# Kernel tuning notes

Hardware: AMD Instinct MI355X
Metric: run time of the kernel (lower is better)

The kernel has to match this reference:

```python
import jax, jax.numpy as jnp
import numpy as np

T, L, B, M, E, H, A, HID, OBS = 8, 2, 512, 128, 512, 8, 16, 1024, 64
DH = E // H


def _ln(x, s, b):
    m = jnp.mean(x, axis=-1, keepdims=True)
    v = jnp.var(x, axis=-1, keepdims=True)
    return (x - m) * jax.lax.rsqrt(v + 1e-6) * s + b


def _mlp(z, w1, b1, w2, b2, w3, b3):
    z = jax.nn.relu(z @ w1 + b1)
    z = jax.nn.relu(z @ w2 + b2)
    return z @ w3 + b3


def setup_inputs() -> dict:
    key = jax.random.key(0)
    ks = jax.random.split(key, 20)
    r = lambda i, shape: jax.random.normal(ks[i], shape, jnp.float32) * 0.02
    return dict(
        memories=jax.random.normal(ks[0], (B, L, M, E), jnp.float32),
        obs=jax.random.normal(ks[1], (B, OBS), jnp.float32),
        We=r(2, (T, OBS, E)), be=jnp.zeros((T, E), jnp.float32),
        Wq=r(3, (T, L, E, E)), Wk=r(4, (T, L, E, E)), Wv=r(5, (T, L, E, E)),
        Wo=r(6, (T, L, E, E)), bo=jnp.zeros((T, L, E), jnp.float32),
        W1=r(7, (T, L, E, E)), b1=jnp.zeros((T, L, E), jnp.float32),
        W2=r(8, (T, L, E, E)), b2=jnp.zeros((T, L, E), jnp.float32),
        ln1_s=jnp.ones((T, L, E), jnp.float32), ln1_b=jnp.zeros((T, L, E), jnp.float32),
        ln2_s=jnp.ones((T, L, E), jnp.float32), ln2_b=jnp.zeros((T, L, E), jnp.float32),
        aW1=r(9, (T, E, HID)), ab1=jnp.zeros((T, HID), jnp.float32),
        aW2=r(10, (T, HID, HID)), ab2=jnp.zeros((T, HID), jnp.float32),
        aW3=r(11, (T, HID, A)), ab3=jnp.zeros((T, A), jnp.float32),
        cW1=r(12, (T, E, HID)), cb1=jnp.zeros((T, HID), jnp.float32),
        cW2=r(13, (T, HID, HID)), cb2=jnp.zeros((T, HID), jnp.float32),
        cW3=r(14, (T, HID, 1)), cb3=jnp.zeros((T, 1), jnp.float32),
        state_skills=jax.random.randint(ks[15], (B,), 0, T),
        mask=jnp.ones((B, M), dtype=bool),
    )


def reference(memories, obs, We, be, Wq, Wk, Wv, Wo, bo, W1, b1, W2, b2,
              ln1_s, ln1_b, ln2_s, ln2_b, aW1, ab1, aW2, ab2, aW3, ab3,
              cW1, cb1, cW2, cb2, cW3, cb3, state_skills, mask):
    scale = 1.0 / np.sqrt(DH)
    # current-step token is always attendable -> append True column
    fmask = jnp.concatenate([mask, jnp.ones((B, 1), dtype=bool)], axis=1)  # [B, M+1]
    xs, mems = [], []
    for t in range(T):  # dense compute over ALL tasks (as in the original)
        h = obs @ We[t] + be[t]  # [B, E]
        layer_mems = []
        for l in range(L):
            layer_mems.append(h)  # TrXL-style: memory_out = layer inputs
            kv = jnp.concatenate([memories[:, l], h[:, None, :]], axis=1)  # [B, M+1, E]
            qn = _ln(h, ln1_s[t, l], ln1_b[t, l])
            kn = _ln(kv, ln1_s[t, l], ln1_b[t, l])
            q = (qn @ Wq[t, l]).reshape(B, H, DH)
            k = (kn @ Wk[t, l]).reshape(B, M + 1, H, DH)
            v = (kn @ Wv[t, l]).reshape(B, M + 1, H, DH)
            s = jnp.einsum('bhd,bshd->bhs', q, k) * scale
            s = jnp.where(fmask[:, None, :], s, -1e9)
            p = jax.nn.softmax(s, axis=-1)
            o = jnp.einsum('bhs,bshd->bhd', p, v).reshape(B, E) @ Wo[t, l] + bo[t, l]
            h = h + o
            hn = _ln(h, ln2_s[t, l], ln2_b[t, l])
            h = h + jax.nn.relu(hn @ W1[t, l] + b1[t, l]) @ W2[t, l] + b2[t, l]
        xs.append(h)
        mems.append(jnp.stack(layer_mems, axis=1))  # [B, L, E]
    x_all = jnp.stack(xs, axis=1)       # [B, T, E]
    mem_all = jnp.stack(mems, axis=1)   # [B, T, L, E]
    onehot = jnp.eye(T, dtype=x_all.dtype)[state_skills]  # [B, T]
    x = jnp.sum(x_all * onehot[:, :, None], axis=1)                 # [B, E]
    memory_out = jnp.sum(mem_all * onehot[:, :, None, None], axis=1)  # [B, L, E]
    actor = jnp.stack([_mlp(x, aW1[t], ab1[t], aW2[t], ab2[t], aW3[t], ab3[t]) for t in range(T)], axis=1)   # [B, T, A]
    critic = jnp.stack([_mlp(x, cW1[t], cb1[t], cW2[t], cb2[t], cW3[t], cb3[t]) for t in range(T)], axis=1)  # [B, T, 1]
    logits = jnp.sum(actor * onehot[:, :, None], axis=1)                    # [B, A]
    values = jnp.sum(critic * onehot[:, :, None], axis=1).squeeze(-1)       # [B]
    return logits, values, memory_out
```

## Files before the change

kernel.cpp:

```cpp
#include <hip/hip_runtime.h>

#define TT    8
#define LLAY  2
#define BB    512
#define MM    128
#define EE    512
#define NH    8
#define HID   1024
#define NA    16
#define NOBS  64

#define OUT_LOGITS 0
#define OUT_VALUES (BB*NA)
#define OUT_MEM    (BB*NA + BB)

#define WS_H    0
#define WS_R    (WS_H + BB*EE)
#define WS_B16  (WS_R + BB*NH*EE)
#define U_QN    0
#define U_HN    (U_QN + BB*EE)
#define U_F1    (U_HN + BB*EE)
#define U_O     (U_F1 + BB*EE)
#define U_HB    (U_O  + BB*EE)
#define U_PV    (U_HB + BB*EE)
#define U_Z1A   (U_PV + BB*NH*EE)
#define U_Z2A   (U_Z1A + BB*HID)
#define U_Z1C   (U_Z2A + BB*HID)
#define U_Z2C   (U_Z1C + BB*HID)
#define U_OBSB  (U_Z2C + BB*HID)
#define U_QB    (U_OBSB + BB*NOBS)
#define U_END   (U_QB + BB*EE)
#define WS_INT  (WS_B16 + (U_END + 1)/2)

#define WI_CNT  0
#define WI_OFF  8
#define WI_MODE 17
#define WI_ROWL 32

typedef __attribute__((ext_vector_type(8))) short bf16x8;
typedef __attribute__((ext_vector_type(4))) float f32x4;

__device__ __forceinline__ unsigned short f2bf(float f) {
  unsigned u = __float_as_uint(f);
  unsigned r = (u + 0x7fffu + ((u >> 16) & 1u)) >> 16;
  return (unsigned short)r;
}
__device__ __forceinline__ float bf2f(unsigned short u) {
  return __uint_as_float(((unsigned)u) << 16);
}
__device__ __forceinline__ float bflo(unsigned u) { return __uint_as_float(u << 16); }
__device__ __forceinline__ float bfhi(unsigned u) { return __uint_as_float(u & 0xffff0000u); }

__device__ __forceinline__ unsigned cvt_pk_bf16(float lo, float hi) {
  unsigned r;
  asm("v_cvt_pk_bf16_f32 %0, %1, %2" : "=v"(r) : "v"(lo), "v"(hi));
  return r;
}
__device__ __forceinline__ bf16x8 pack8(const float* f) {
  union { unsigned u[4]; bf16x8 v; } x;
  x.u[0] = cvt_pk_bf16(f[0], f[1]);
  x.u[1] = cvt_pk_bf16(f[2], f[3]);
  x.u[2] = cvt_pk_bf16(f[4], f[5]);
  x.u[3] = cvt_pk_bf16(f[6], f[7]);
  return x.v;
}

#define DPP_ADD(x, ctrl) \
  (x) += __int_as_float(__builtin_amdgcn_update_dpp(0, __float_as_int(x), (ctrl), 0xf, 0xf, true))

__device__ __forceinline__ float wave_sum(float x) {
  DPP_ADD(x, 0x121);
  DPP_ADD(x, 0x122);
  DPP_ADD(x, 0x124);
  DPP_ADD(x, 0x128);
  x += __shfl_xor(x, 16);
  x += __shfl_xor(x, 32);
  return x;
}

__device__ __forceinline__ float f4c(const float4 v, int c) {
  return c == 0 ? v.x : (c == 1 ? v.y : (c == 2 ? v.z : v.w));
}

__global__ __launch_bounds__(256) void prep_k(const int* __restrict__ skills,
                                              const void* __restrict__ mask,
                                              const float* __restrict__ obs,
                                              unsigned short* __restrict__ obsb,
                                              int* __restrict__ wsI)
{
  if (blockIdx.x > 0) {
    const int i = ((blockIdx.x - 1)*256 + threadIdx.x)*4;
    const float4 v = *(const float4*)(obs + i);
    uint2 p;
    p.x = cvt_pk_bf16(v.x, v.y);
    p.y = cvt_pk_bf16(v.z, v.w);
    *(uint2*)(obsb + i) = p;
    return;
  }
  __shared__ int cnt_s[TT];
  __shared__ int off_s[TT];
  const int tid = threadIdx.x;
  if (tid < TT) cnt_s[tid] = 0;
  __syncthreads();
  const int b0 = tid, b1i = tid + 256;
  const int t0 = skills[b0], t1 = skills[b1i];
  const int o0 = atomicAdd(&cnt_s[t0], 1);
  const int o1 = atomicAdd(&cnt_s[t1], 1);
  __syncthreads();
  if (tid == 0) {
    int off = 0;
    for (int t = 0; t < TT; ++t) {
      off_s[t] = off;
      wsI[WI_CNT + t] = cnt_s[t];
      wsI[WI_OFF + t] = off;
      off += cnt_s[t];
    }
    const unsigned char* m8 = (const unsigned char*)mask;
    const int w0 = *(const int*)mask;
    int mode = 0;
    if (m8[0] == 1 && m8[1] == 1 && m8[2] == 1 && m8[3] == 1) mode = 0;
    else if (w0 == 1) mode = 1;
    else if (w0 == 0x3f800000) mode = 2;
    wsI[WI_MODE] = mode;
  }
  __syncthreads();
  wsI[WI_ROWL + off_s[t0] + o0] = b0;
  wsI[WI_ROWL + off_s[t1] + o1] = b1i;
}

template<bool MEMOUT>
__global__ __launch_bounds__(256) void ln_k(const float* __restrict__ src,
                                            unsigned short* __restrict__ dst,
                                            const float* __restrict__ sp,
                                            const float* __restrict__ bp,
                                            const int* __restrict__ skills,
                                            float* __restrict__ memout, int l)
{
  const int b = blockIdx.x, tid = threadIdx.x;
  const int t = skills[b];
  const float x0 = src[(size_t)b*EE + tid];
  const float x1 = src[(size_t)b*EE + tid + 256];
  if (MEMOUT) {
    memout[((size_t)b*LLAY + l)*EE + tid] = x0;
    memout[((size_t)b*LLAY + l)*EE + tid + 256] = x1;
  }
  __shared__ float rs[4], rq[4];
  float s = wave_sum(x0 + x1);
  float q = wave_sum(x0*x0 + x1*x1);
  const int wvi = tid >> 6, lane = tid & 63;
  if (lane == 0) { rs[wvi] = s; rq[wvi] = q; }
  __syncthreads();
  const float S = rs[0] + rs[1] + rs[2] + rs[3];
  const float Q = rq[0] + rq[1] + rq[2] + rq[3];
  const float mu = S * (1.f/EE);
  const float inv = rsqrtf(Q*(1.f/EE) - mu*mu + 1e-6f);
  const size_t pb = ((size_t)t*LLAY + l)*EE;
  dst[(size_t)b*EE + tid]       = f2bf((x0 - mu)*inv*sp[pb + tid]       + bp[pb + tid]);
  dst[(size_t)b*EE + tid + 256] = f2bf((x1 - mu)*inv*sp[pb + tid + 256] + bp[pb + tid + 256]);
}

template<int KK, int KSPLIT, int RF, bool RELU, bool HASBIAS, bool HASRES, bool OUTBF, bool HEADA, bool OUTBOTH>
__global__ __launch_bounds__((KSPLIT == 8) ? 512 : 256) void mg_k(
    const unsigned short* __restrict__ Aa, const unsigned short* __restrict__ Ab, int lda,
    const float* __restrict__ Wa, const float* __restrict__ Wb, long wStride, long wOff,
    int N,
    const float* __restrict__ biasa, const float* __restrict__ biasb, int bStride, int bOff,
    const float* __restrict__ res, int ldres,
    void* __restrict__ Ca, void* __restrict__ Cb_, int ldc,
    unsigned short* __restrict__ C2,
    const int* __restrict__ wsI)
{
  constexpr int NW = (KSPLIT == 8) ? 8 : 4;
  constexpr int Kper = KK / KSPLIT;
  constexpr int NK = Kper / 32;
  constexpr int MR = RF * 16;
  const int t = blockIdx.z & 7, sel = blockIdx.z >> 3;
  const int cnt = wsI[WI_CNT + t];
  if (cnt == 0) return;
  const int* rowl = wsI + WI_ROWL + wsI[WI_OFF + t];
  const int tid = threadIdx.x, lane = tid & 63, w = tid >> 6;
  const int l15 = lane & 15, l4 = lane >> 4;
  const int kw    = (KSPLIT == 8) ? w : (w & 1);
  const int ntile = (KSPLIT == 8) ? 0 : (w >> 1);
  const int jbase = blockIdx.x * (KSPLIT == 8 ? 16 : 32) + ntile*16;

  const unsigned short* A = sel ? Ab : Aa;
  const float* Wt = (sel ? Wb : Wa) + (size_t)t*wStride + wOff;
  const float* wp = Wt + (size_t)(kw*Kper + l4*8)*N + jbase + l15;

  bf16x8 afr[NK];
  #pragma unroll
  for (int kk = 0; kk < NK; ++kk) {
    float f[8];
    #pragma unroll
    for (int j = 0; j < 8; ++j) f[j] = wp[(size_t)(kk*32 + j)*N];
    afr[kk] = pack8(f);
  }

  __shared__ __align__(16) f32x4 red_s[NW][RF][64];

  for (int rb = blockIdx.y*MR; rb < cnt; rb += (int)gridDim.y*MR) {
    int row[RF];
    const unsigned short* ap[RF];
    #pragma unroll
    for (int rf = 0; rf < RF; ++rf) {
      row[rf] = rowl[min(rb + rf*16 + l15, cnt - 1)];
      ap[rf] = A + (size_t)row[rf]*lda
          + (HEADA ? (size_t)(jbase >> 6)*EE : 0) + kw*Kper + l4*8;
    }
    f32x4 acc[RF];
    #pragma unroll
    for (int rf = 0; rf < RF; ++rf) acc[rf] = (f32x4){0.f, 0.f, 0.f, 0.f};

    #pragma unroll
    for (int kk = 0; kk < NK; ++kk) {
      #pragma unroll
      for (int rf = 0; rf < RF; ++rf) {
        const bf16x8 bfr = *(const bf16x8*)(ap[rf] + kk*32);
        acc[rf] = __builtin_amdgcn_mfma_f32_16x16x32_bf16(afr[kk], bfr, acc[rf], 0, 0, 0);
      }
    }

    #pragma unroll
    for (int rf = 0; rf < RF; ++rf) red_s[w][rf][lane] = acc[rf];
    __syncthreads();

    if (kw == 0) {
      #pragma unroll
      for (int rf = 0; rf < RF; ++rf) {
        if (KSPLIT == 8) {
          #pragma unroll
          for (int ww = 1; ww < 8; ++ww) acc[rf] += red_s[ww][rf][lane];
        } else {
          acc[rf] += red_s[w + 1][rf][lane];
        }
        if (rb + rf*16 + l15 < cnt) {
          const int nb = jbase + l4*4;
          float vv[4];
          float4 bv, rv;
          if (HASBIAS) bv = *(const float4*)((sel ? biasb : biasa) + (size_t)t*bStride + bOff + nb);
          if (HASRES)  rv = *(const float4*)(res + (size_t)row[rf]*ldres + nb);
          #pragma unroll
          for (int c = 0; c < 4; ++c) {
            float x = acc[rf][c];
            if (HASBIAS) x += f4c(bv, c);
            if (RELU)    x = fmaxf(x, 0.f);
            if (HASRES)  x += f4c(rv, c);
            vv[c] = x;
          }
          void* C = sel ? Cb_ : Ca;
          if (OUTBF) {
            uint2 p;
            p.x = cvt_pk_bf16(vv[0], vv[1]);
            p.y = cvt_pk_bf16(vv[2], vv[3]);
            *(uint2*)((unsigned short*)C + (size_t)row[rf]*ldc + nb) = p;
          } else {
            *(float4*)((float*)C + (size_t)row[rf]*ldc + nb) = make_float4(vv[0], vv[1], vv[2], vv[3]);
          }
          if (OUTBOTH) {
            uint2 p;
            p.x = cvt_pk_bf16(vv[0], vv[1]);
            p.y = cvt_pk_bf16(vv[2], vv[3]);
            *(uint2*)(C2 + (size_t)row[rf]*ldc + nb) = p;
          }
        }
      }
    }
    __syncthreads();
  }
}

__global__ __launch_bounds__(256) void rk_k(const unsigned short* __restrict__ qb,
                                            const float* __restrict__ Wk,
                                            float* __restrict__ R_ws,
                                            const int* __restrict__ wsI, int l)
{
  const int t = blockIdx.z & 7, h = blockIdx.z >> 3;
  const int cnt = wsI[WI_CNT + t];
  if (cnt == 0) return;
  const int* rowl = wsI + WI_ROWL + wsI[WI_OFF + t];
  const int tid = threadIdx.x, lane = tid & 63, w = tid >> 6;
  const int l15 = lane & 15, l4 = lane >> 4;
  const int kw = w & 1, ntile = w >> 1;
  const int ebase = blockIdx.x*32 + ntile*16;

  const float* wp = Wk + ((size_t)t*LLAY + l)*EE*EE
      + (size_t)(ebase + l15)*EE + h*64 + kw*32 + l4*8;

  __shared__ __align__(16) f32x4 red_s[4][2][64];

  for (int rb = blockIdx.y*32; rb < cnt; rb += (int)gridDim.y*32) {
    int row[2];
    const unsigned short* ap[2];
    #pragma unroll
    for (int rf = 0; rf < 2; ++rf) {
      row[rf] = rowl[min(rb + rf*16 + l15, cnt - 1)];
      ap[rf] = qb + (size_t)row[rf]*EE + h*64 + kw*32 + l4*8;
    }
    float f[8];
    *(float4*)&f[0] = *(const float4*)wp;
    *(float4*)&f[4] = *(const float4*)(wp + 4);
    const bf16x8 afr = pack8(f);
    f32x4 acc[2];
    #pragma unroll
    for (int rf = 0; rf < 2; ++rf) {
      const bf16x8 bfr = *(const bf16x8*)ap[rf];
      acc[rf] = __builtin_amdgcn_mfma_f32_16x16x32_bf16(afr, bfr,
                  (f32x4){0.f,0.f,0.f,0.f}, 0, 0, 0);
    }
    #pragma unroll
    for (int rf = 0; rf < 2; ++rf) red_s[w][rf][lane] = acc[rf];
    __syncthreads();
    if (kw == 0) {
      #pragma unroll
      for (int rf = 0; rf < 2; ++rf) {
        acc[rf] += red_s[w + 1][rf][lane];
        if (rb + rf*16 + l15 < cnt) {
          const int e = ebase + l4*4;
          *(float4*)(R_ws + ((size_t)row[rf]*NH + h)*EE + e) =
              make_float4(acc[rf][0], acc[rf][1], acc[rf][2], acc[rf][3]);
        }
      }
    }
    __syncthreads();
  }
}

__global__ __launch_bounds__(256) void attn_k(const float* __restrict__ mem,
                                              const unsigned short* __restrict__ qn,
                                              const float* __restrict__ R_ws,
                                              const float* __restrict__ ln1s,
                                              const float* __restrict__ ln1b,
                                              const void* __restrict__ mask,
                                              const int* __restrict__ skills,
                                              const int* __restrict__ wsI,
                                              unsigned short* __restrict__ PV, int l)
{
  const int b = blockIdx.x, tid = threadIdx.x;
  const int wvi = tid >> 6, lane = tid & 63;
  const int l15 = lane & 15, l4 = lane >> 4;
  const int t = skills[b];
  const int mode = wsI[WI_MODE];

  __shared__ __align__(16) float qn_l[EE];
  __shared__ __align__(16) float w_s[NH][132];
  __shared__ __align__(16) float p_s[NH][MM];
  __shared__ float mu_s[MM], inv_s[MM], S_s[MM], Q_s[MM];
  __shared__ float hsS[NH], hsA[NH], hsP[NH], hspex[NH];
  __shared__ __align__(16) unsigned short rp_bf[16][520];
  __shared__ __align__(16) float score_s[MM][20];

  for (int i = tid; i < EE; i += 256) qn_l[i] = bf2f(qn[(size_t)b*EE + i]);

  const int e8 = lane*8;
  const float* s1p = ln1s + ((size_t)t*LLAY + l)*EE;
  const float* b1p = ln1b + ((size_t)t*LLAY + l)*EE;
  float s1v[8], b1v[8], qnv[8];
  *(float4*)&s1v[0] = *(const float4*)(s1p + e8);
  *(float4*)&s1v[4] = *(const float4*)(s1p + e8 + 4);
  *(float4*)&b1v[0] = *(const float4*)(b1p + e8);
  *(float4*)&b1v[4] = *(const float4*)(b1p + e8 + 4);
  {
    const uint4 qu = *(const uint4*)(qn + (size_t)b*EE + e8);
    qnv[0] = bflo(qu.x); qnv[1] = bfhi(qu.x);
    qnv[2] = bflo(qu.y); qnv[3] = bfhi(qu.y);
    qnv[4] = bflo(qu.z); qnv[5] = bfhi(qu.z);
    qnv[6] = bflo(qu.w); qnv[7] = bfhi(qu.w);
  }

  const float scale = 0.125f;
  float rp[NH][8];
  float SR[NH], BR[NH], SE[NH];
  #pragma unroll
  for (int h = 0; h < NH; ++h) {
    float rv[8];
    *(float4*)&rv[0] = *(const float4*)(R_ws + ((size_t)b*NH + h)*EE + e8);
    *(float4*)&rv[4] = *(const float4*)(R_ws + ((size_t)b*NH + h)*EE + e8 + 4);
    float pr = 0.f, pb = 0.f, ps = 0.f;
    #pragma unroll
    for (int j = 0; j < 8; ++j) {
      const float r = rv[j]*scale;
      const float x = r*s1v[j];
      rp[h][j] = x;
      pr += x; pb += b1v[j]*r; ps += qnv[j]*r;
    }
    SR[h] = wave_sum(pr);
    BR[h] = wave_sum(pb);
    SE[h] = wave_sum(ps);
  }

  if (wvi == 0) {
    #pragma unroll
    for (int h = 0; h < NH; ++h)
      *(bf16x8*)&rp_bf[h][e8] = pack8(rp[h]);
  } else if (wvi == 1) {
    bf16x8 ones, zer;
    #pragma unroll
    for (int j = 0; j < 8; ++j) { ones[j] = (short)0x3F80; zer[j] = 0; }
    *(bf16x8*)&rp_bf[8][e8] = ones;
    #pragma unroll
    for (int r = 9; r < 16; ++r) *(bf16x8*)&rp_bf[r][e8] = zer;
  }
  if (tid == 0) {
    #pragma unroll
    for (int h = 0; h < NH; ++h) w_s[h][MM] = SE[h];
  }
  __syncthreads();

  const float* base = mem + ((size_t)b*LLAY + l)*MM*EE;
  #pragma unroll
  for (int half = 0; half < 2; ++half) {
    const int mt = wvi + half*4;
    const int mg = mt*16 + l15;
    const float* xp = base + (size_t)mg*EE + l4*8;
    f32x4 sacc = {0.f,0.f,0.f,0.f}, gacc = {0.f,0.f,0.f,0.f};
    #pragma unroll
    for (int ks = 0; ks < 16; ++ks) {
      float f[8];
      *(float4*)&f[0] = *(const float4*)(xp + ks*32);
      *(float4*)&f[4] = *(const float4*)(xp + ks*32 + 4);
      const bf16x8 xfr = pack8(f);
      const bf16x8 afr = *(const bf16x8*)&rp_bf[l15][ks*32 + l4*8];
      sacc = __builtin_amdgcn_mfma_f32_16x16x32_bf16(afr, xfr, sacc, 0, 0, 0);
      gacc = __builtin_amdgcn_mfma_f32_16x16x32_bf16(xfr, xfr, gacc, 0, 0, 0);
    }
    if (l4 < 2) *(f32x4*)&score_s[mg][l4*4] = sacc;
    if (l4 == 2) S_s[mg] = sacc[0];
    if (l4 == (l15 >> 2)) {
      const int c = l15 & 3;
      Q_s[mg] = (c == 0) ? gacc[0] : (c == 1) ? gacc[1] : (c == 2) ? gacc[2] : gacc[3];
    }
  }
  __syncthreads();

  if (tid < MM) {
    const int m = tid;
    const float muv = S_s[m]*(1.f/EE);
    const float invv = rsqrtf(Q_s[m]*(1.f/EE) - muv*muv + 1e-6f);
    mu_s[m] = muv; inv_s[m] = invv;
    bool valid;
    if (mode == 0)      valid = ((const unsigned char*)mask)[(size_t)b*MM + m] != 0;
    else if (mode == 1) valid = ((const int*)mask)[(size_t)b*MM + m] != 0;
    else                valid = ((const float*)mask)[(size_t)b*MM + m] != 0.f;
    #pragma unroll
    for (int h = 0; h < NH; ++h) {
      const float sc = invv*score_s[m][h] - muv*invv*SR[h] + BR[h];
      const float p = valid ? __expf(sc) : 0.f;
      p_s[h][m] = p;
      w_s[h][m] = p*invv;
    }
  }
  __syncthreads();

  {
    const int h = tid >> 5, li = tid & 31;
    const float p0 = p_s[h][li], p1 = p_s[h][li+32], p2 = p_s[h][li+64], p3 = p_s[h][li+96];
    const float i0 = inv_s[li], i1 = inv_s[li+32], i2 = inv_s[li+64], i3 = inv_s[li+96];
    const float m0 = mu_s[li], m1 = mu_s[li+32], m2 = mu_s[li+64], m3 = mu_s[li+96];
    const float pe = (li == 0) ? __expf(w_s[h][MM]) : 0.f;
    float Sp = p0 + p1 + p2 + p3 + pe;
    float Ap = p0*m0*i0 + p1*m1*i1 + p2*m2*i2 + p3*m3*i3;
    float Pp = p0 + p1 + p2 + p3;
    #pragma unroll
    for (int o = 16; o; o >>= 1) {
      Sp += __shfl_xor(Sp, o);
      Ap += __shfl_xor(Ap, o);
      Pp += __shfl_xor(Pp, o);
    }
    if (li == 0) { hsS[h] = Sp; hsA[h] = Ap; hsP[h] = Pp; hspex[h] = pe; }
  }
  __syncthreads();

  const int e0 = wvi*128 + lane*2;
  const float s1x = s1p[e0], s1y = s1p[e0+1];
  const float b1x = b1p[e0], b1y = b1p[e0+1];
  const float qx = qn_l[e0], qy = qn_l[e0+1];
  float accx[NH], accy[NH];
  #pragma unroll
  for (int h = 0; h < NH; ++h) { accx[h] = 0.f; accy[h] = 0.f; }
  const float* bp2 = mem + ((size_t)b*LLAY + l)*MM*EE + e0;
  for (int m4 = 0; m4 < MM; m4 += 4) {
    float4 wv4[NH];
    #pragma unroll
    for (int h = 0; h < NH; ++h) wv4[h] = *(const float4*)&w_s[h][m4];
    #pragma unroll
    for (int c = 0; c < 4; ++c) {
      const float2 x2 = *(const float2*)(bp2 + (size_t)(m4 + c)*EE);
      #pragma unroll
      for (int h = 0; h < NH; ++h) {
        const float wv = f4c(wv4[h], c);
        accx[h] += wv*x2.x;
        accy[h] += wv*x2.y;
      }
    }
  }
  #pragma unroll
  for (int h = 0; h < NH; ++h) {
    const float is = 1.f/hsS[h];
    const float px = (s1x*(accx[h] - hsA[h]) + b1x*hsP[h] + hspex[h]*qx)*is;
    const float py = (s1y*(accy[h] - hsA[h]) + b1y*hsP[h] + hspex[h]*qy)*is;
    const unsigned pk = cvt_pk_bf16(px, py);
    *(unsigned*)(PV + ((size_t)b*NH + h)*EE + e0) = pk;
  }
}

__global__ __launch_bounds__(256) void head_k(const unsigned short* __restrict__ z2a,
                                              const unsigned short* __restrict__ z2c,
                                              const float* __restrict__ aW3,
                                              const float* __restrict__ ab3,
                                              const float* __restrict__ cW3,
                                              const float* __restrict__ cb3,
                                              const int* __restrict__ skills,
                                              float* __restrict__ out)
{
  const int b = blockIdx.x, tid = threadIdx.x;
  const int t = skills[b];
  __shared__ float za[HID], zc[HID];
  __shared__ float red[16][17];
  __shared__ float redv[4];
  for (int i = tid; i < HID; i += 256) {
    za[i] = bf2f(z2a[(size_t)b*HID + i]);
    zc[i] = bf2f(z2c[(size_t)b*HID + i]);
  }
  __syncthreads();
  {
    const int j = tid & 15, grp = tid >> 4;
    const float* w = aW3 + (size_t)t*HID*NA;
    float p = 0.f;
    for (int i = grp*64; i < grp*64 + 64; ++i) p += za[i]*w[(size_t)i*NA + j];
    red[grp][j] = p;
  }
  float pvv = 0.f;
  {
    const float* w = cW3 + (size_t)t*HID;
    for (int i = tid; i < HID; i += 256) pvv += zc[i]*w[i];
  }
  pvv = wave_sum(pvv);
  const int wvi = tid >> 6, lane = tid & 63;
  if (lane == 0) redv[wvi] = pvv;
  __syncthreads();
  if (tid < 16) {
    float v = ab3[(size_t)t*NA + tid];
    #pragma unroll
    for (int g = 0; g < 16; ++g) v += red[g][tid];
    out[OUT_LOGITS + (size_t)b*NA + tid] = v;
  }
  if (tid == 0)
    out[OUT_VALUES + b] = cb3[t] + redv[0] + redv[1] + redv[2] + redv[3];
}

extern "C" void kernel_launch(void* const* d_in, const int* in_sizes, int n_in,
                              void* d_out, int out_size, void* d_ws, size_t ws_size,
                              hipStream_t stream)
{
  (void)in_sizes; (void)n_in; (void)out_size; (void)ws_size;
  const float* memories = (const float*)d_in[0];
  const float* obs   = (const float*)d_in[1];
  const float* We    = (const float*)d_in[2];
  const float* be    = (const float*)d_in[3];
  const float* Wq    = (const float*)d_in[4];
  const float* Wk    = (const float*)d_in[5];
  const float* Wv    = (const float*)d_in[6];
  const float* Wo    = (const float*)d_in[7];
  const float* bo    = (const float*)d_in[8];
  const float* W1    = (const float*)d_in[9];
  const float* b1    = (const float*)d_in[10];
  const float* W2    = (const float*)d_in[11];
  const float* b2    = (const float*)d_in[12];
  const float* ln1s  = (const float*)d_in[13];
  const float* ln1b  = (const float*)d_in[14];
  const float* ln2s  = (const float*)d_in[15];
  const float* ln2b  = (const float*)d_in[16];
  const float* aW1   = (const float*)d_in[17];
  const float* ab1   = (const float*)d_in[18];
  const float* aW2   = (const float*)d_in[19];
  const float* ab2   = (const float*)d_in[20];
  const float* aW3   = (const float*)d_in[21];
  const float* ab3   = (const float*)d_in[22];
  const float* cW1   = (const float*)d_in[23];
  const float* cb1   = (const float*)d_in[24];
  const float* cW2   = (const float*)d_in[25];
  const float* cb2   = (const float*)d_in[26];
  const float* cW3   = (const float*)d_in[27];
  const float* cb3   = (const float*)d_in[28];
  const int*   skills= (const int*)d_in[29];
  const void*  mask  = d_in[30];

  float* ws  = (float*)d_ws;
  float* out = (float*)d_out;
  float* h   = ws + WS_H;
  float* R   = ws + WS_R;
  unsigned short* bf = (unsigned short*)(ws + WS_B16);
  unsigned short* qn   = bf + U_QN;
  unsigned short* hn   = bf + U_HN;
  unsigned short* f1   = bf + U_F1;
  unsigned short* o    = bf + U_O;
  unsigned short* hb   = bf + U_HB;
  unsigned short* PV   = bf + U_PV;
  unsigned short* z1a  = bf + U_Z1A;
  unsigned short* z2a  = bf + U_Z2A;
  unsigned short* z1c  = bf + U_Z1C;
  unsigned short* z2c  = bf + U_Z2C;
  unsigned short* obsb = bf + U_OBSB;
  unsigned short* qb   = bf + U_QB;
  int* wsI = (int*)(ws + WS_INT);

  prep_k<<<1 + BB*NOBS/1024, 256, 0, stream>>>(skills, mask, obs, obsb, wsI);

  mg_k<64,2,2,false,true,false,false,false,false><<<dim3(EE/32,4,TT), 256, 0, stream>>>(
      obsb, obsb, NOBS, We, We, (long)NOBS*EE, 0, EE,
      be, be, EE, 0, nullptr, 0, h, h, EE, nullptr, wsI);

  for (int l = 0; l < LLAY; ++l) {
    const long wOff = (long)l*EE*EE;
    ln_k<true><<<BB, 256, 0, stream>>>(h, qn, ln1s, ln1b, skills, out + OUT_MEM, l);
    mg_k<512,8,2,false,false,false,true,false,false><<<dim3(EE/16,2,TT), 512, 0, stream>>>(
        qn, qn, EE, Wq, Wq, (long)LLAY*EE*EE, wOff, EE,
        nullptr, nullptr, 0, 0, nullptr, 0, qb, qb, EE, nullptr, wsI);
    rk_k<<<dim3(EE/32,2,TT*NH), 256, 0, stream>>>(qb, Wk, R, wsI, l);
    attn_k<<<BB, 256, 0, stream>>>(memories, qn, R, ln1s, ln1b, mask, skills, wsI, PV, l);
    mg_k<512,8,2,false,false,false,true,true,false><<<dim3(EE/16,2,TT), 512, 0, stream>>>(
        PV, PV, NH*EE, Wv, Wv, (long)LLAY*EE*EE, wOff, EE,
        nullptr, nullptr, 0, 0, nullptr, 0, o, o, EE, nullptr, wsI);
    mg_k<512,8,2,false,true,true,false,false,false><<<dim3(EE/16,2,TT), 512, 0, stream>>>(
        o, o, EE, Wo, Wo, (long)LLAY*EE*EE, wOff, EE,
        bo, bo, LLAY*EE, l*EE, h, EE, h, h, EE, nullptr, wsI);
    ln_k<false><<<BB, 256, 0, stream>>>(h, hn, ln2s, ln2b, skills, nullptr, l);
    mg_k<512,8,2,true,true,false,true,false,false><<<dim3(EE/16,2,TT), 512, 0, stream>>>(
        hn, hn, EE, W1, W1, (long)LLAY*EE*EE, wOff, EE,
        b1, b1, LLAY*EE, l*EE, nullptr, 0, f1, f1, EE, nullptr, wsI);
    if (l == LLAY - 1) {
      mg_k<512,8,2,false,true,true,false,false,true><<<dim3(EE/16,2,TT), 512, 0, stream>>>(
          f1, f1, EE, W2, W2, (long)LLAY*EE*EE, wOff, EE,
          b2, b2, LLAY*EE, l*EE, h, EE, h, h, EE, hb, wsI);
    } else {
      mg_k<512,8,2,false,true,true,false,false,false><<<dim3(EE/16,2,TT), 512, 0, stream>>>(
          f1, f1, EE, W2, W2, (long)LLAY*EE*EE, wOff, EE,
          b2, b2, LLAY*EE, l*EE, h, EE, h, h, EE, nullptr, wsI);
    }
  }

  mg_k<512,8,4,true,true,false,true,false,false><<<dim3(HID/16,1,2*TT), 512, 0, stream>>>(
      hb, hb, EE, aW1, cW1, (long)EE*HID, 0, HID,
      ab1, cb1, HID, 0, nullptr, 0, z1a, z1c, HID, nullptr, wsI);
  mg_k<1024,8,4,true,true,false,true,false,false><<<dim3(HID/16,1,2*TT), 512, 0, stream>>>(
      z1a, z1c, HID, aW2, cW2, (long)HID*HID, 0, HID,
      ab2, cb2, HID, 0, nullptr, 0, z2a, z2c, HID, nullptr, wsI);

  head_k<<<BB, 256, 0, stream>>>(z2a, z2c, aW3, ab3, cW3, cb3, skills, out);
}
```

Baseline: 305.6 us.

## Fuse LayerNorm into GEMM prologues and attention kernel, drop ln_k launches

```diff
diff --git a/kernel.cpp b/kernel.cpp
--- a/kernel.cpp
+++ b/kernel.cpp
@@ -17,9 +17,7 @@
 #define WS_H    0
 #define WS_R    (WS_H + BB*EE)
 #define WS_B16  (WS_R + BB*NH*EE)
-#define U_QN    0
-#define U_HN    (U_QN + BB*EE)
-#define U_F1    (U_HN + BB*EE)
+#define U_F1    0
 #define U_O     (U_F1 + BB*EE)
 #define U_HB    (U_O  + BB*EE)
 #define U_PV    (U_HB + BB*EE)
@@ -40,17 +38,9 @@
 typedef __attribute__((ext_vector_type(8))) short bf16x8;
 typedef __attribute__((ext_vector_type(4))) float f32x4;
 
-__device__ __forceinline__ unsigned short f2bf(float f) {
-  unsigned u = __float_as_uint(f);
-  unsigned r = (u + 0x7fffu + ((u >> 16) & 1u)) >> 16;
-  return (unsigned short)r;
-}
 __device__ __forceinline__ float bf2f(unsigned short u) {
   return __uint_as_float(((unsigned)u) << 16);
 }
-__device__ __forceinline__ float bflo(unsigned u) { return __uint_as_float(u << 16); }
-__device__ __forceinline__ float bfhi(unsigned u) { return __uint_as_float(u & 0xffff0000u); }
-
 __device__ __forceinline__ unsigned cvt_pk_bf16(float lo, float hi) {
   unsigned r;
   asm("v_cvt_pk_bf16_f32 %0, %1, %2" : "=v"(r) : "v"(lo), "v"(hi));
@@ -128,46 +118,15 @@
   wsI[WI_ROWL + off_s[t1] + o1] = b1i;
 }
 
-template<bool MEMOUT>
-__global__ __launch_bounds__(256) void ln_k(const float* __restrict__ src,
-                                            unsigned short* __restrict__ dst,
-                                            const float* __restrict__ sp,
-                                            const float* __restrict__ bp,
-                                            const int* __restrict__ skills,
-                                            float* __restrict__ memout, int l)
-{
-  const int b = blockIdx.x, tid = threadIdx.x;
-  const int t = skills[b];
-  const float x0 = src[(size_t)b*EE + tid];
-  const float x1 = src[(size_t)b*EE + tid + 256];
-  if (MEMOUT) {
-    memout[((size_t)b*LLAY + l)*EE + tid] = x0;
-    memout[((size_t)b*LLAY + l)*EE + tid + 256] = x1;
-  }
-  __shared__ float rs[4], rq[4];
-  float s = wave_sum(x0 + x1);
-  float q = wave_sum(x0*x0 + x1*x1);
-  const int wvi = tid >> 6, lane = tid & 63;
-  if (lane == 0) { rs[wvi] = s; rq[wvi] = q; }
-  __syncthreads();
-  const float S = rs[0] + rs[1] + rs[2] + rs[3];
-  const float Q = rq[0] + rq[1] + rq[2] + rq[3];
-  const float mu = S * (1.f/EE);
-  const float inv = rsqrtf(Q*(1.f/EE) - mu*mu + 1e-6f);
-  const size_t pb = ((size_t)t*LLAY + l)*EE;
-  dst[(size_t)b*EE + tid]       = f2bf((x0 - mu)*inv*sp[pb + tid]       + bp[pb + tid]);
-  dst[(size_t)b*EE + tid + 256] = f2bf((x1 - mu)*inv*sp[pb + tid + 256] + bp[pb + tid + 256]);
-}
-
-template<int KK, int KSPLIT, int RF, bool RELU, bool HASBIAS, bool HASRES, bool OUTBF, bool HEADA, bool OUTBOTH>
+template<int KK, int KSPLIT, int RF, bool LNIN, bool RELU, bool HASBIAS, bool HASRES, bool OUTBF, bool HEADA>
 __global__ __launch_bounds__((KSPLIT == 8) ? 512 : 256) void mg_k(
-    const unsigned short* __restrict__ Aa, const unsigned short* __restrict__ Ab, int lda,
+    const void* __restrict__ Aa, const void* __restrict__ Ab, int lda,
     const float* __restrict__ Wa, const float* __restrict__ Wb, long wStride, long wOff,
     int N,
     const float* __restrict__ biasa, const float* __restrict__ biasb, int bStride, int bOff,
+    const float* __restrict__ lnS, const float* __restrict__ lnB, long lnOff,
     const float* __restrict__ res, int ldres,
     void* __restrict__ Ca, void* __restrict__ Cb_, int ldc,
-    unsigned short* __restrict__ C2,
     const int* __restrict__ wsI)
 {
   constexpr int NW = (KSPLIT == 8) ? 8 : 4;
@@ -184,7 +143,6 @@
   const int ntile = (KSPLIT == 8) ? 0 : (w >> 1);
   const int jbase = blockIdx.x * (KSPLIT == 8 ? 16 : 32) + ntile*16;
 
-  const unsigned short* A = sel ? Ab : Aa;
   const float* Wt = (sel ? Wb : Wa) + (size_t)t*wStride + wOff;
   const float* wp = Wt + (size_t)(kw*Kper + l4*8)*N + jbase + l15;
 
@@ -197,29 +155,90 @@
     afr[kk] = pack8(f);
   }
 
+  float s1v[NK][8], b1v[NK][8];
+  if constexpr (LNIN) {
+    const float* sp = lnS + (size_t)t*(LLAY*EE) + lnOff + kw*Kper + l4*8;
+    const float* bp = lnB + (size_t)t*(LLAY*EE) + lnOff + kw*Kper + l4*8;
+    #pragma unroll
+    for (int kk = 0; kk < NK; ++kk) {
+      *(float4*)&s1v[kk][0] = *(const float4*)(sp + kk*32);
+      *(float4*)&s1v[kk][4] = *(const float4*)(sp + kk*32 + 4);
+      *(float4*)&b1v[kk][0] = *(const float4*)(bp + kk*32);
+      *(float4*)&b1v[kk][4] = *(const float4*)(bp + kk*32 + 4);
+    }
+  }
+
   __shared__ __align__(16) f32x4 red_s[NW][RF][64];
+  __shared__ float2 lnred_s[8][RF][16];
 
   for (int rb = blockIdx.y*MR; rb < cnt; rb += (int)gridDim.y*MR) {
     int row[RF];
-    const unsigned short* ap[RF];
+    size_t abase[RF];
     #pragma unroll
     for (int rf = 0; rf < RF; ++rf) {
       row[rf] = rowl[min(rb + rf*16 + l15, cnt - 1)];
-      ap[rf] = A + (size_t)row[rf]*lda
+      abase[rf] = (size_t)row[rf]*lda
           + (HEADA ? (size_t)(jbase >> 6)*EE : 0) + kw*Kper + l4*8;
     }
-    f32x4 acc[RF];
-    #pragma unroll
-    for (int rf = 0; rf < RF; ++rf) acc[rf] = (f32x4){0.f, 0.f, 0.f, 0.f};
-
-    #pragma unroll
-    for (int kk = 0; kk < NK; ++kk) {
+
+    bf16x8 bfrv[RF][NK];
+    if constexpr (LNIN) {
+      float av[RF][NK][8];
       #pragma unroll
       for (int rf = 0; rf < RF; ++rf) {
-        const bf16x8 bfr = *(const bf16x8*)(ap[rf] + kk*32);
-        acc[rf] = __builtin_amdgcn_mfma_f32_16x16x32_bf16(afr[kk], bfr, acc[rf], 0, 0, 0);
+        const float* apf = (const float*)(sel ? Ab : Aa) + abase[rf];
+        float s = 0.f, q = 0.f;
+        #pragma unroll
+        for (int kk = 0; kk < NK; ++kk) {
+          *(float4*)&av[rf][kk][0] = *(const float4*)(apf + kk*32);
+          *(float4*)&av[rf][kk][4] = *(const float4*)(apf + kk*32 + 4);
+          #pragma unroll
+          for (int j = 0; j < 8; ++j) {
+            s += av[rf][kk][j];
+            q += av[rf][kk][j]*av[rf][kk][j];
+          }
+        }
+        s += __shfl_xor(s, 16); s += __shfl_xor(s, 32);
+        q += __shfl_xor(q, 16); q += __shfl_xor(q, 32);
+        if (l4 == 0) lnred_s[w][rf][l15] = make_float2(s, q);
       }
-    }
+      __syncthreads();
+      #pragma unroll
+      for (int rf = 0; rf < RF; ++rf) {
+        float S = 0.f, Q = 0.f;
+        #pragma unroll
+        for (int ww = 0; ww < NW; ++ww) {
+          const float2 v = lnred_s[ww][rf][l15];
+          S += v.x; Q += v.y;
+        }
+        const float mu = S*(1.f/EE);
+        const float inv = rsqrtf(Q*(1.f/EE) - mu*mu + 1e-6f);
+        #pragma unroll
+        for (int kk = 0; kk < NK; ++kk) {
+          float f[8];
+          #pragma unroll
+          for (int j = 0; j < 8; ++j)
+            f[j] = (av[rf][kk][j] - mu)*inv*s1v[kk][j] + b1v[kk][j];
+          bfrv[rf][kk] = pack8(f);
+        }
+      }
+    } else {
+      #pragma unroll
+      for (int rf = 0; rf < RF; ++rf)
+        #pragma unroll
+        for (int kk = 0; kk < NK; ++kk)
+          bfrv[rf][kk] = *(const bf16x8*)((const unsigned short*)(sel ? Ab : Aa)
+                                          + abase[rf] + kk*32);
+    }
+
+    f32x4 acc[RF];
+    #pragma unroll
+    for (int rf = 0; rf < RF; ++rf) acc[rf] = (f32x4){0.f, 0.f, 0.f, 0.f};
+    #pragma unroll
+    for (int kk = 0; kk < NK; ++kk)
+      #pragma unroll
+      for (int rf = 0; rf < RF; ++rf)
+        acc[rf] = __builtin_amdgcn_mfma_f32_16x16x32_bf16(afr[kk], bfrv[rf][kk], acc[rf], 0, 0, 0);
 
     #pragma unroll
     for (int rf = 0; rf < RF; ++rf) red_s[w][rf][lane] = acc[rf];
@@ -257,12 +276,6 @@
           } else {
             *(float4*)((float*)C + (size_t)row[rf]*ldc + nb) = make_float4(vv[0], vv[1], vv[2], vv[3]);
           }
-          if (OUTBOTH) {
-            uint2 p;
-            p.x = cvt_pk_bf16(vv[0], vv[1]);
-            p.y = cvt_pk_bf16(vv[2], vv[3]);
-            *(uint2*)(C2 + (size_t)row[rf]*ldc + nb) = p;
-          }
         }
       }
     }
@@ -286,25 +299,20 @@
 
   const float* wp = Wk + ((size_t)t*LLAY + l)*EE*EE
       + (size_t)(ebase + l15)*EE + h*64 + kw*32 + l4*8;
+  float f[8];
+  *(float4*)&f[0] = *(const float4*)wp;
+  *(float4*)&f[4] = *(const float4*)(wp + 4);
+  const bf16x8 afr = pack8(f);
 
   __shared__ __align__(16) f32x4 red_s[4][2][64];
 
-  for (int rb = blockIdx.y*32; rb < cnt; rb += (int)gridDim.y*32) {
+  for (int rb = 0; rb < cnt; rb += 32) {
     int row[2];
-    const unsigned short* ap[2];
+    f32x4 acc[2];
     #pragma unroll
     for (int rf = 0; rf < 2; ++rf) {
       row[rf] = rowl[min(rb + rf*16 + l15, cnt - 1)];
-      ap[rf] = qb + (size_t)row[rf]*EE + h*64 + kw*32 + l4*8;
-    }
-    float f[8];
-    *(float4*)&f[0] = *(const float4*)wp;
-    *(float4*)&f[4] = *(const float4*)(wp + 4);
-    const bf16x8 afr = pack8(f);
-    f32x4 acc[2];
-    #pragma unroll
-    for (int rf = 0; rf < 2; ++rf) {
-      const bf16x8 bfr = *(const bf16x8*)ap[rf];
+      const bf16x8 bfr = *(const bf16x8*)(qb + (size_t)row[rf]*EE + h*64 + kw*32 + l4*8);
       acc[rf] = __builtin_amdgcn_mfma_f32_16x16x32_bf16(afr, bfr,
                   (f32x4){0.f,0.f,0.f,0.f}, 0, 0, 0);
     }
@@ -327,14 +335,15 @@
 }
 
 __global__ __launch_bounds__(256) void attn_k(const float* __restrict__ mem,
-                                              const unsigned short* __restrict__ qn,
+                                              const float* __restrict__ hsrc,
                                               const float* __restrict__ R_ws,
                                               const float* __restrict__ ln1s,
                                               const float* __restrict__ ln1b,
                                               const void* __restrict__ mask,
                                               const int* __restrict__ skills,
                                               const int* __restrict__ wsI,
-                                              unsigned short* __restrict__ PV, int l)
+                                              unsigned short* __restrict__ PV,
+                                              float* __restrict__ memout, int l)
 {
   const int b = blockIdx.x, tid = threadIdx.x;
   const int wvi = tid >> 6, lane = tid & 63;
@@ -349,24 +358,37 @@
   __shared__ float hsS[NH], hsA[NH], hsP[NH], hspex[NH];
   __shared__ __align__(16) unsigned short rp_bf[16][520];
   __shared__ __align__(16) float score_s[MM][20];
-
-  for (int i = tid; i < EE; i += 256) qn_l[i] = bf2f(qn[(size_t)b*EE + i]);
-
-  const int e8 = lane*8;
+  __shared__ float rs_s[4], rq_s[4];
+
   const float* s1p = ln1s + ((size_t)t*LLAY + l)*EE;
   const float* b1p = ln1b + ((size_t)t*LLAY + l)*EE;
+
+  {
+    const float* hr = hsrc + (size_t)b*EE;
+    const float x0 = hr[tid], x1 = hr[tid + 256];
+    memout[((size_t)b*LLAY + l)*EE + tid] = x0;
+    memout[((size_t)b*LLAY + l)*EE + tid + 256] = x1;
+    float s = wave_sum(x0 + x1);
+    float q = wave_sum(x0*x0 + x1*x1);
+    if (lane == 0) { rs_s[wvi] = s; rq_s[wvi] = q; }
+    __syncthreads();
+    const float S = rs_s[0] + rs_s[1] + rs_s[2] + rs_s[3];
+    const float Q = rq_s[0] + rq_s[1] + rq_s[2] + rq_s[3];
+    const float mu = S*(1.f/EE);
+    const float inv = rsqrtf(Q*(1.f/EE) - mu*mu + 1e-6f);
+    qn_l[tid]       = (x0 - mu)*inv*s1p[tid]       + b1p[tid];
+    qn_l[tid + 256] = (x1 - mu)*inv*s1p[tid + 256] + b1p[tid + 256];
+  }
+  __syncthreads();
+
+  const int e8 = lane*8;
   float s1v[8], b1v[8], qnv[8];
   *(float4*)&s1v[0] = *(const float4*)(s1p + e8);
   *(float4*)&s1v[4] = *(const float4*)(s1p + e8 + 4);
   *(float4*)&b1v[0] = *(const float4*)(b1p + e8);
   *(float4*)&b1v[4] = *(const float4*)(b1p + e8 + 4);
-  {
-    const uint4 qu = *(const uint4*)(qn + (size_t)b*EE + e8);
-    qnv[0] = bflo(qu.x); qnv[1] = bfhi(qu.x);
-    qnv[2] = bflo(qu.y); qnv[3] = bfhi(qu.y);
-    qnv[4] = bflo(qu.z); qnv[5] = bfhi(qu.z);
-    qnv[6] = bflo(qu.w); qnv[7] = bfhi(qu.w);
-  }
+  *(float4*)&qnv[0] = *(const float4*)&qn_l[e8];
+  *(float4*)&qnv[4] = *(const float4*)&qn_l[e8 + 4];
 
   const float scale = 0.125f;
   float rp[NH][8];
@@ -591,8 +613,6 @@
   float* h   = ws + WS_H;
   float* R   = ws + WS_R;
   unsigned short* bf = (unsigned short*)(ws + WS_B16);
-  unsigned short* qn   = bf + U_QN;
-  unsigned short* hn   = bf + U_HN;
   unsigned short* f1   = bf + U_F1;
   unsigned short* o    = bf + U_O;
   unsigned short* hb   = bf + U_HB;
@@ -607,45 +627,44 @@
 
   prep_k<<<1 + BB*NOBS/1024, 256, 0, stream>>>(skills, mask, obs, obsb, wsI);
 
-  mg_k<64,2,2,false,true,false,false,false,false><<<dim3(EE/32,4,TT), 256, 0, stream>>>(
+  mg_k<64,2,2,false,false,true,false,false,false><<<dim3(EE/32,4,TT), 256, 0, stream>>>(
       obsb, obsb, NOBS, We, We, (long)NOBS*EE, 0, EE,
-      be, be, EE, 0, nullptr, 0, h, h, EE, nullptr, wsI);
+      be, be, EE, 0, nullptr, nullptr, 0, nullptr, 0, h, h, EE, wsI);
 
   for (int l = 0; l < LLAY; ++l) {
     const long wOff = (long)l*EE*EE;
-    ln_k<true><<<BB, 256, 0, stream>>>(h, qn, ln1s, ln1b, skills, out + OUT_MEM, l);
-    mg_k<512,8,2,false,false,false,true,false,false><<<dim3(EE/16,2,TT), 512, 0, stream>>>(
-        qn, qn, EE, Wq, Wq, (long)LLAY*EE*EE, wOff, EE,
-        nullptr, nullptr, 0, 0, nullptr, 0, qb, qb, EE, nullptr, wsI);
-    rk_k<<<dim3(EE/32,2,TT*NH), 256, 0, stream>>>(qb, Wk, R, wsI, l);
-    attn_k<<<BB, 256, 0, stream>>>(memories, qn, R, ln1s, ln1b, mask, skills, wsI, PV, l);
-    mg_k<512,8,2,false,false,false,true,true,false><<<dim3(EE/16,2,TT), 512, 0, stream>>>(
+    mg_k<512,8,2,true,false,false,false,true,false><<<dim3(EE/16,2,TT), 512, 0, stream>>>(
+        h, h, EE, Wq, Wq, (long)LLAY*EE*EE, wOff, EE,
+        nullptr, nullptr, 0, 0, ln1s, ln1b, (long)l*EE, nullptr, 0, qb, qb, EE, wsI);
+    rk_k<<<dim3(EE/32,1,TT*NH), 256, 0, stream>>>(qb, Wk, R, wsI, l);
+    attn_k<<<BB, 256, 0, stream>>>(memories, h, R, ln1s, ln1b, mask, skills, wsI,
+                                   PV, out + OUT_MEM, l);
+    mg_k<512,8,2,false,false,false,false,true,true><<<dim3(EE/16,2,TT), 512, 0, stream>>>(
         PV, PV, NH*EE, Wv, Wv, (long)LLAY*EE*EE, wOff, EE,
-        nullptr, nullptr, 0, 0, nullptr, 0, o, o, EE, nullptr, wsI);
-    mg_k<512,8,2,false,true,true,false,false,false><<<dim3(EE/16,2,TT), 512, 0, stream>>>(
+        nullptr, nullptr, 0, 0, nullptr, nullptr, 0, nullptr, 0, o, o, EE, wsI);
+    mg_k<512,8,2,false,false,true,true,false,false><<<dim3(EE/16,2,TT), 512, 0, stream>>>(
         o, o, EE, Wo, Wo, (long)LLAY*EE*EE, wOff, EE,
-        bo, bo, LLAY*EE, l*EE, h, EE, h, h, EE, nullptr, wsI);
-    ln_k<false><<<BB, 256, 0, stream>>>(h, hn, ln2s, ln2b, skills, nullptr, l);
-    mg_k<512,8,2,true,true,false,true,false,false><<<dim3(EE/16,2,TT), 512, 0, stream>>>(
-        hn, hn, EE, W1, W1, (long)LLAY*EE*EE, wOff, EE,
-        b1, b1, LLAY*EE, l*EE, nullptr, 0, f1, f1, EE, nullptr, wsI);
+        bo, bo, LLAY*EE, l*EE, nullptr, nullptr, 0, h, EE, h, h, EE, wsI);
+    mg_k<512,8,2,true,true,true,false,true,false><<<dim3(EE/16,2,TT), 512, 0, stream>>>(
+        h, h, EE, W1, W1, (long)LLAY*EE*EE, wOff, EE,
+        b1, b1, LLAY*EE, l*EE, ln2s, ln2b, (long)l*EE, nullptr, 0, f1, f1, EE, wsI);
     if (l == LLAY - 1) {
-      mg_k<512,8,2,false,true,true,false,false,true><<<dim3(EE/16,2,TT), 512, 0, stream>>>(
+      mg_k<512,8,2,false,false,true,true,true,false><<<dim3(EE/16,2,TT), 512, 0, stream>>>(
           f1, f1, EE, W2, W2, (long)LLAY*EE*EE, wOff, EE,
-          b2, b2, LLAY*EE, l*EE, h, EE, h, h, EE, hb, wsI);
+          b2, b2, LLAY*EE, l*EE, nullptr, nullptr, 0, h, EE, hb, hb, EE, wsI);
     } else {
-      mg_k<512,8,2,false,true,true,false,false,false><<<dim3(EE/16,2,TT), 512, 0, stream>>>(
+      mg_k<512,8,2,false,false,true,true,false,false><<<dim3(EE/16,2,TT), 512, 0, stream>>>(
           f1, f1, EE, W2, W2, (long)LLAY*EE*EE, wOff, EE,
-          b2, b2, LLAY*EE, l*EE, h, EE, h, h, EE, nullptr, wsI);
-    }
-  }
-
-  mg_k<512,8,4,true,true,false,true,false,false><<<dim3(HID/16,1,2*TT), 512, 0, stream>>>(
+          b2, b2, LLAY*EE, l*EE, nullptr, nullptr, 0, h, EE, h, h, EE, wsI);
+    }
+  }
+
+  mg_k<512,8,4,false,true,true,false,true,false><<<dim3(HID/16,1,2*TT), 512, 0, stream>>>(
       hb, hb, EE, aW1, cW1, (long)EE*HID, 0, HID,
-      ab1, cb1, HID, 0, nullptr, 0, z1a, z1c, HID, nullptr, wsI);
-  mg_k<1024,8,4,true,true,false,true,false,false><<<dim3(HID/16,1,2*TT), 512, 0, stream>>>(
+      ab1, cb1, HID, 0, nullptr, nullptr, 0, nullptr, 0, z1a, z1c, HID, wsI);
+  mg_k<1024,8,4,false,true,true,false,true,false><<<dim3(HID/16,1,2*TT), 512, 0, stream>>>(
       z1a, z1c, HID, aW2, cW2, (long)HID*HID, 0, HID,
-      ab2, cb2, HID, 0, nullptr, 0, z2a, z2c, HID, nullptr, wsI);
+      ab2, cb2, HID, 0, nullptr, nullptr, 0, nullptr, 0, z2a, z2c, HID, wsI);
 
   head_k<<<BB, 256, 0, stream>>>(z2a, z2c, aW3, ab3, cW3, cb3, skills, out);
 }
```

After: 312.8 us. 2.4% more time.
